# Optimization experiments

Hardware: AMD Instinct MI355X
Metric: run time of the kernel (lower is better)

The kernel has to match this reference:

```python
import jax, jax.numpy as jnp
import numpy as np

B, N, D, H = 2, 2048, 1024, 16
DK = D // H


def setup_inputs() -> dict:
    key = jax.random.key(0)
    ks = jax.random.split(key, 12)
    s = D ** -0.5
    inp = {
        "query": jax.random.normal(ks[0], (B, N, D), jnp.float32),
        "key": jax.random.normal(ks[1], (B, N, D), jnp.float32),
        "value": jax.random.normal(ks[2], (B, N, D), jnp.float32),
        # causal mask: 1 = keep, 0 = masked (matches create_causal_mask)
        "mask": jnp.tril(jnp.ones((N, N), jnp.int32)),
        "Wq": jax.random.normal(ks[3], (D, D), jnp.float32) * s,
        "bq": jnp.zeros((D,), jnp.float32),
        "Wk": jax.random.normal(ks[4], (D, D), jnp.float32) * s,
        "bk": jnp.zeros((D,), jnp.float32),
        "Wv": jax.random.normal(ks[5], (D, D), jnp.float32) * s,
        "bv": jnp.zeros((D,), jnp.float32),
        "Wo": jax.random.normal(ks[6], (D, D), jnp.float32) * s,
        "bo": jnp.zeros((D,), jnp.float32),
    }
    return inp


def reference(query, key, value, mask, Wq, bq, Wk, bk, Wv, bv, Wo, bo):
    scale = DK ** -0.5
    # Linear projections (torch nn.Linear: x @ W.T + b), split into heads -> [B,H,N,DK]
    q = (query @ Wq.T + bq).reshape(B, N, H, DK).transpose(0, 2, 1, 3)
    k = (key @ Wk.T + bk).reshape(B, N, H, DK).transpose(0, 2, 1, 3)
    v = (value @ Wv.T + bv).reshape(B, N, H, DK).transpose(0, 2, 1, 3)
    scores = jnp.einsum("bhqd,bhkd->bhqk", q, k) * scale  # [B,H,N,N]
    scores = jnp.where(mask[None, None, :, :] == 0, jnp.float32(-1e9), scores)
    attn = jax.nn.softmax(scores, axis=-1)
    ctx = jnp.einsum("bhqk,bhkd->bhqd", attn, v)  # [B,H,N,DK]
    ctx = ctx.transpose(0, 2, 1, 3).reshape(B, N, D)
    return ctx @ Wo.T + bo
```

## Files before the change

### kernel.cpp

```cpp
#include <hip/hip_runtime.h>
#include <hip/hip_bf16.h>

typedef __attribute__((ext_vector_type(4))) float f32x4;
typedef __attribute__((ext_vector_type(8))) __bf16 bf16x8;
typedef __attribute__((ext_vector_type(8))) unsigned short u16x8;
typedef __attribute__((ext_vector_type(4))) unsigned short u16x4;
typedef unsigned short u16;

#define DEV static __device__ __forceinline__

DEV u16 f2bf(float f){
  unsigned u = __builtin_bit_cast(unsigned, f);
  u += 0x7fff + ((u >> 16) & 1);
  return (u16)(u >> 16);
}

DEV f32x4 mfma16(bf16x8 a, bf16x8 b, f32x4 c){
  return __builtin_amdgcn_mfma_f32_16x16x32_bf16(a, b, c, 0, 0, 0);
}

DEV void gload16(const void* g, void* l){
  __builtin_amdgcn_global_load_lds((const __attribute__((address_space(1))) void*)g,
                                   (__attribute__((address_space(3))) void*)l,
                                   16, 0, 0);
}

__global__ __launch_bounds__(256) void cvt_k(
    const float* __restrict__ s0, const float* __restrict__ s1,
    const float* __restrict__ s2, const float* __restrict__ s3,
    const float* __restrict__ s4, const float* __restrict__ s5,
    const float* __restrict__ s6,
    u16* __restrict__ d0, u16* __restrict__ d1, u16* __restrict__ d2,
    u16* __restrict__ d3, u16* __restrict__ d4, u16* __restrict__ d5,
    u16* __restrict__ d6){
  const int y = blockIdx.y;
  const float* __restrict__ s = y==0?s0:y==1?s1:y==2?s2:y==3?s3:y==4?s4:y==5?s5:s6;
  u16* __restrict__ d         = y==0?d0:y==1?d1:y==2?d2:y==3?d3:y==4?d4:y==5?d5:d6;
  const int n8 = (y < 3) ? (4096*1024/8) : (1024*1024/8);
  for (int i = blockIdx.x*256 + threadIdx.x; i < n8; i += gridDim.x*256){
    f32x4 a = *(const f32x4*)&s[(size_t)i*8];
    f32x4 b = *(const f32x4*)&s[(size_t)i*8 + 4];
    u16x8 h;
    #pragma unroll
    for (int j = 0; j < 4; ++j){ h[j] = f2bf(a[j]); h[j+4] = f2bf(b[j]); }
    *(u16x8*)&d[(size_t)i*8] = h;
  }
}

template<int OUT_F32>
__global__ __launch_bounds__(256) void gemm_bt(
    const u16* __restrict__ A0, const u16* __restrict__ A1, const u16* __restrict__ A2,
    const u16* __restrict__ B0, const u16* __restrict__ B1, const u16* __restrict__ B2,
    const float* __restrict__ e0, const float* __restrict__ e1, const float* __restrict__ e2,
    void* __restrict__ C0, void* __restrict__ C1, void* __restrict__ C2){
  __shared__ u16 As[128*32];
  __shared__ u16 Bs[128*32];
  const int z = blockIdx.z;
  const u16* __restrict__ A    = z==0 ? A0 : z==1 ? A1 : A2;
  const u16* __restrict__ Bw   = z==0 ? B0 : z==1 ? B1 : B2;
  const float* __restrict__ bias = z==0 ? e0 : z==1 ? e1 : e2;
  void* __restrict__ Cp        = z==0 ? C0 : z==1 ? C1 : C2;
  const bool vt = (OUT_F32 == 0) && (z == 2);

  const int tid  = threadIdx.x;
  const int lane = tid & 63, w = tid >> 6;
  const int wr = w >> 1, wc = w & 1;
  const int l16 = lane & 15, lhi = lane >> 4;
  const int bm = vt ? blockIdx.x : blockIdx.y;
  const int bn = vt ? blockIdx.y : blockIdx.x;

  const int srow = w*16 + (lane >> 2);
  const int scol = (lane & 3)*8;
  const u16* Asrc = A  + (size_t)(bm*128 + srow)*1024 + scol;
  const u16* Bsrc = Bw + (size_t)(bn*128 + srow)*1024 + scol;
  u16* Adst0 = As + w*512;
  u16* Bdst0 = Bs + w*512;

  f32x4 acc[4][4] = {};

  for (int k0 = 0; k0 < 1024; k0 += 32){
    __syncthreads();
    gload16(Asrc + k0,             Adst0);
    gload16(Asrc + 64*1024 + k0,   Adst0 + 2048);
    gload16(Bsrc + k0,             Bdst0);
    gload16(Bsrc + 64*1024 + k0,   Bdst0 + 2048);
    __syncthreads();

    bf16x8 af[4], bfr[4];
    #pragma unroll
    for (int mi = 0; mi < 4; ++mi)
      af[mi] = *(const bf16x8*)&As[(wr*64 + mi*16 + l16)*32 + lhi*8];
    #pragma unroll
    for (int nf = 0; nf < 4; ++nf)
      bfr[nf] = *(const bf16x8*)&Bs[(wc*64 + nf*16 + l16)*32 + lhi*8];
    #pragma unroll
    for (int mi = 0; mi < 4; ++mi)
      #pragma unroll
      for (int nf = 0; nf < 4; ++nf)
        acc[mi][nf] = mfma16(af[mi], bfr[nf], acc[mi][nf]);
  }

  #pragma unroll
  for (int mi = 0; mi < 4; ++mi){
    #pragma unroll
    for (int nf = 0; nf < 4; ++nf){
      int row0 = bm*128 + wr*64 + mi*16 + lhi*4;
      int col  = bn*128 + wc*64 + nf*16 + l16;
      float bc = bias[col];
      #pragma unroll
      for (int r = 0; r < 4; ++r){
        int row = row0 + r;
        float val = acc[mi][nf][r] + (vt ? bias[row] : bc);
        if (OUT_F32){
          ((float*)Cp)[(size_t)row*1024 + col] = val;
        } else if (!vt){
          int b = row >> 11, n = row & 2047;
          int h = col >> 6,  dk = col & 63;
          ((u16*)Cp)[(((size_t)(b*16 + h))*2048 + n)*64 + dk] = f2bf(val);
        } else {
          int h = row >> 6,  dk = row & 63;
          int b = col >> 11, n = col & 2047;
          ((u16*)Cp)[(((size_t)(b*16 + h))*64 + dk)*2048 + n] = f2bf(val);
        }
      }
    }
  }
}

__global__ __launch_bounds__(256) void attn_k(const u16* __restrict__ Q,
                                              const u16* __restrict__ K,
                                              const u16* __restrict__ Vt,
                                              u16* __restrict__ CTX){
  __shared__ u16 Ks[64*64];
  __shared__ u16 Vs[64*64];
  __shared__ u16 Ps[4][16][72];
  const int tid  = threadIdx.x;
  const int lane = tid & 63, w = tid >> 6;
  const int l16 = lane & 15, lhi = lane >> 4;
  const int f  = blockIdx.x;
  const int bh = f & 31, xp = f >> 5;
  const size_t base = (size_t)bh * 2048 * 64;
  const u16* Qb = Q  + base;
  const u16* Kb = K  + base;
  const u16* Vb = Vt + base;
  const int b = bh >> 4, h = bh & 15;

  const int s0 = tid, s1 = tid + 256;
  const int r0 = s0 >> 3, c0 = ((s0 & 7) ^ (r0 & 7))*8;
  const int r1 = s1 >> 3, c1 = ((s1 & 7) ^ (r1 & 7))*8;
  const u16* Ksrc0 = Kb + r0*64 + c0;
  const u16* Ksrc1 = Kb + r1*64 + c1;
  const u16* Vsrc0 = Vb + (size_t)r0*2048 + c0;
  const u16* Vsrc1 = Vb + (size_t)r1*2048 + c1;
  u16* Kdst0 = Ks + s0*8;  u16* Kdst1 = Ks + s1*8;
  u16* Vdst0 = Vs + s0*8;  u16* Vdst1 = Vs + s1*8;
  const int swz = (l16 & 7)*8;

  #pragma unroll
  for (int half = 0; half < 2; ++half){
    const int qt = half == 0 ? xp : 31 - xp;
    const int q0 = qt * 64;
    const int q_abs = q0 + w*16 + l16;

    bf16x8 bq[2];
    #pragma unroll
    for (int ks = 0; ks < 2; ++ks)
      bq[ks] = *(const bf16x8*)&Qb[(size_t)q_abs*64 + ks*32 + lhi*8];

    f32x4 ctx[4] = {};
    float m_r = -3.0e38f, l_r = 0.f;

    const int nt = qt + 1;
    for (int t = 0; t < nt; ++t){
      __syncthreads();
      gload16(Ksrc0 + t*4096, Kdst0);
      gload16(Ksrc1 + t*4096, Kdst1);
      gload16(Vsrc0 + t*64,   Vdst0);
      gload16(Vsrc1 + t*64,   Vdst1);
      __syncthreads();

      f32x4 s4[4] = {};
      #pragma unroll
      for (int nf = 0; nf < 4; ++nf)
        #pragma unroll
        for (int ks = 0; ks < 2; ++ks){
          bf16x8 ak = *(const bf16x8*)&Ks[(nf*16 + l16)*64 + ((ks*32 + lhi*8) ^ swz)];
          s4[nf] = mfma16(ak, bq[ks], s4[nf]);
        }

      float mt = -3.0e38f;
      #pragma unroll
      for (int nf = 0; nf < 4; ++nf)
        #pragma unroll
        for (int r = 0; r < 4; ++r){
          float x = s4[nf][r] * 0.125f;
          int kc = t*64 + nf*16 + lhi*4 + r;
          x = (kc > q_abs) ? -1.0e30f : x;
          s4[nf][r] = x;
          mt = fmaxf(mt, x);
        }
      mt = fmaxf(mt, __shfl_xor(mt, 16));
      mt = fmaxf(mt, __shfl_xor(mt, 32));
      float mn = fmaxf(m_r, mt);
      float sf = __expf(m_r - mn);
      m_r = mn;

      float lt = 0.f;
      #pragma unroll
      for (int nf = 0; nf < 4; ++nf){
        u16x4 hq;
        #pragma unroll
        for (int r = 0; r < 4; ++r){
          float p = __expf(s4[nf][r] - mn);
          lt += p;
          hq[r] = f2bf(p);
        }
        *(u16x4*)&Ps[w][l16][nf*16 + lhi*4] = hq;
      }
      lt += __shfl_xor(lt, 16);
      lt += __shfl_xor(lt, 32);
      l_r = l_r * sf + lt;

      float sfb[4];
      #pragma unroll
      for (int r = 0; r < 4; ++r)
        sfb[r] = __shfl(sf, (lane >> 4)*4 + r);
      #pragma unroll
      for (int dkf = 0; dkf < 4; ++dkf)
        #pragma unroll
        for (int r = 0; r < 4; ++r)
          ctx[dkf][r] *= sfb[r];

      #pragma unroll
      for (int ks = 0; ks < 2; ++ks){
        bf16x8 pa = *(const bf16x8*)&Ps[w][l16][ks*32 + lhi*8];
        #pragma unroll
        for (int dkf = 0; dkf < 4; ++dkf){
          bf16x8 vb = *(const bf16x8*)&Vs[(dkf*16 + l16)*64 + ((ks*32 + lhi*8) ^ swz)];
          ctx[dkf] = mfma16(pa, vb, ctx[dkf]);
        }
      }
    }

    float lf[4];
    #pragma unroll
    for (int r = 0; r < 4; ++r)
      lf[r] = __shfl(l_r, (lane >> 4)*4 + r);
    #pragma unroll
    for (int dkf = 0; dkf < 4; ++dkf)
      #pragma unroll
      for (int r = 0; r < 4; ++r){
        int q = q0 + w*16 + lhi*4 + r;
        float val = ctx[dkf][r] / lf[r];
        CTX[((size_t)(b*2048 + q))*1024 + h*64 + dkf*16 + l16] = f2bf(val);
      }
  }
}

constexpr int LDP = 40;

__global__ __launch_bounds__(256) void gemm_qkv(
    const float* __restrict__ Aq, const float* __restrict__ Ak, const float* __restrict__ Av,
    const float* __restrict__ Bq, const float* __restrict__ Bk, const float* __restrict__ Bv,
    const float* __restrict__ eq, const float* __restrict__ ek, const float* __restrict__ ev,
    u16* __restrict__ Oq, u16* __restrict__ Ok, u16* __restrict__ Ov){
  __shared__ u16 As[128][LDP];
  __shared__ u16 Bs[128][LDP];
  const int z = blockIdx.z;
  const float* __restrict__ A   = z == 0 ? Aq : z == 1 ? Ak : Av;
  const float* __restrict__ W   = z == 0 ? Bq : z == 1 ? Bk : Bv;
  const float* __restrict__ bias= z == 0 ? eq : z == 1 ? ek : ev;
  u16* __restrict__ C           = z == 0 ? Oq : z == 1 ? Ok : Ov;
  const bool vt = (z == 2);

  const int tid  = threadIdx.x;
  const int lane = tid & 63, wv = tid >> 6;
  const int wr = wv >> 1, wc = wv & 1;
  const int l16 = lane & 15, lhi = lane >> 4;
  const int bm = vt ? blockIdx.x : blockIdx.y;
  const int bn = vt ? blockIdx.y : blockIdx.x;
  const int K = 1024;

  f32x4 acc[4][4] = {};

  for (int k0 = 0; k0 < K; k0 += 32){
    __syncthreads();
    #pragma unroll
    for (int j = 0; j < 4; ++j){
      int s = tid + j*256;
      int row = s >> 3, c4 = s & 7;
      f32x4 v = *(const f32x4*)&A[(size_t)(bm*128 + row)*K + k0 + c4*4];
      u16x4 hh;
      #pragma unroll
      for (int i = 0; i < 4; ++i) hh[i] = f2bf(v[i]);
      *(u16x4*)&As[row][c4*4] = hh;
    }
    #pragma unroll
    for (int j = 0; j < 4; ++j){
      int s = tid + j*256;
      int row = s >> 3, c4 = s & 7;
      f32x4 v = *(const f32x4*)&W[(size_t)(bn*128 + row)*K + k0 + c4*4];
      u16x4 hh;
      #pragma unroll
      for (int i = 0; i < 4; ++i) hh[i] = f2bf(v[i]);
      *(u16x4*)&Bs[row][c4*4] = hh;
    }
    __syncthreads();

    bf16x8 af[4], bfr[4];
    #pragma unroll
    for (int mi = 0; mi < 4; ++mi)
      af[mi] = *(const bf16x8*)&As[wr*64 + mi*16 + l16][lhi*8];
    #pragma unroll
    for (int nf = 0; nf < 4; ++nf)
      bfr[nf] = *(const bf16x8*)&Bs[wc*64 + nf*16 + l16][lhi*8];
    #pragma unroll
    for (int mi = 0; mi < 4; ++mi)
      #pragma unroll
      for (int nf = 0; nf < 4; ++nf)
        acc[mi][nf] = mfma16(af[mi], bfr[nf], acc[mi][nf]);
  }

  #pragma unroll
  for (int mi = 0; mi < 4; ++mi){
    #pragma unroll
    for (int nf = 0; nf < 4; ++nf){
      int row0 = bm*128 + wr*64 + mi*16 + lhi*4;
      int col  = bn*128 + wc*64 + nf*16 + l16;
      float bc = bias[col];
      #pragma unroll
      for (int r = 0; r < 4; ++r){
        int row = row0 + r;
        float val = acc[mi][nf][r] + (vt ? bias[row] : bc);
        if (!vt){
          int b = row >> 11, n = row & 2047;
          int h = col >> 6,  dk = col & 63;
          C[(((size_t)(b*16 + h))*2048 + n)*64 + dk] = f2bf(val);
        } else {
          int h = row >> 6,  dk = row & 63;
          int b = col >> 11, n = col & 2047;
          C[(((size_t)(b*16 + h))*64 + dk)*2048 + n] = f2bf(val);
        }
      }
    }
  }
}

__global__ __launch_bounds__(256) void gemm_o_fb(const u16* __restrict__ A,
                                                 const float* __restrict__ W,
                                                 const float* __restrict__ bias,
                                                 float* __restrict__ C){
  __shared__ u16 As[128][LDP];
  __shared__ u16 Bs[64][LDP];
  const int tid  = threadIdx.x;
  const int lane = tid & 63, wv = tid >> 6;
  const int wr = wv >> 1, wc = wv & 1;
  const int l16 = lane & 15, lhi = lane >> 4;
  const int bm = blockIdx.y, bn = blockIdx.x;
  const int K = 1024;

  f32x4 acc[4][2] = {};

  for (int k0 = 0; k0 < K; k0 += 32){
    __syncthreads();
    #pragma unroll
    for (int j = 0; j < 2; ++j){
      int s = tid + j*256;
      int row = s >> 2, c8 = s & 3;
      *(u16x8*)&As[row][c8*8] =
          *(const u16x8*)&A[(size_t)(bm*128 + row)*K + k0 + c8*8];
    }
    #pragma unroll
    for (int j = 0; j < 2; ++j){
      int s = tid + j*256;
      int row = s >> 3, c4 = s & 7;
      f32x4 v = *(const f32x4*)&W[(size_t)(bn*64 + row)*K + k0 + c4*4];
      u16x4 hh;
      #pragma unroll
      for (int i = 0; i < 4; ++i) hh[i] = f2bf(v[i]);
      *(u16x4*)&Bs[row][c4*4] = hh;
    }
    __syncthreads();

    bf16x8 af[4], bfr[2];
    #pragma unroll
    for (int mi = 0; mi < 4; ++mi)
      af[mi] = *(const bf16x8*)&As[wr*64 + mi*16 + l16][lhi*8];
    #pragma unroll
    for (int nf = 0; nf < 2; ++nf)
      bfr[nf] = *(const bf16x8*)&Bs[wc*32 + nf*16 + l16][lhi*8];
    #pragma unroll
    for (int mi = 0; mi < 4; ++mi)
      #pragma unroll
      for (int nf = 0; nf < 2; ++nf)
        acc[mi][nf] = mfma16(af[mi], bfr[nf], acc[mi][nf]);
  }

  #pragma unroll
  for (int mi = 0; mi < 4; ++mi){
    #pragma unroll
    for (int nf = 0; nf < 2; ++nf){
      int row0 = bm*128 + wr*64 + mi*16 + lhi*4;
      int col  = bn*64 + wc*32 + nf*16 + l16;
      float bv = bias[col];
      #pragma unroll
      for (int r = 0; r < 4; ++r)
        C[(size_t)(row0 + r)*1024 + col] = acc[mi][nf][r] + bv;
    }
  }
}

extern "C" void kernel_launch(void* const* d_in, const int* in_sizes, int n_in,
                              void* d_out, int out_size, void* d_ws, size_t ws_size,
                              hipStream_t stream){
  const float* q  = (const float*)d_in[0];
  const float* k  = (const float*)d_in[1];
  const float* v  = (const float*)d_in[2];
  const float* Wq = (const float*)d_in[4];  const float* bq = (const float*)d_in[5];
  const float* Wk = (const float*)d_in[6];  const float* bk = (const float*)d_in[7];
  const float* Wv = (const float*)d_in[8];  const float* bv = (const float*)d_in[9];
  const float* Wo = (const float*)d_in[10]; const float* bo = (const float*)d_in[11];
  float* out = (float*)d_out;
  dim3 blk(256);

  const size_t need = (size_t)(3*4194304 + 4*1048576 + 3*4194304) * 2;
  if (ws_size >= need){
    u16* Xqb = (u16*)d_ws;
    u16* Xkb = Xqb + 4194304;
    u16* Xvb = Xkb + 4194304;
    u16* Wqb = Xvb + 4194304;
    u16* Wkb = Wqb + 1048576;
    u16* Wvb = Wkb + 1048576;
    u16* Wob = Wvb + 1048576;
    u16* Qw  = Wob + 1048576;
    u16* Kw  = Qw + 4194304;
    u16* Vw  = Kw + 4194304;
    u16* Cw  = Xqb;

    cvt_k<<<dim3(512, 7), blk, 0, stream>>>(q, k, v, Wq, Wk, Wv, Wo,
                                            Xqb, Xkb, Xvb, Wqb, Wkb, Wvb, Wob);
    gemm_bt<0><<<dim3(8, 32, 3), blk, 0, stream>>>(
        Xqb, Xkb, Wvb, Wqb, Wkb, Xvb, bq, bk, bv,
        (void*)Qw, (void*)Kw, (void*)Vw);
    attn_k<<<dim3(512), blk, 0, stream>>>(Qw, Kw, Vw, Cw);
    gemm_bt<1><<<dim3(8, 32, 1), blk, 0, stream>>>(
        Cw, Cw, Cw, Wob, Wob, Wob, bo, bo, bo,
        (void*)out, (void*)out, (void*)out);
  } else {
    u16* Qw = (u16*)d_ws;
    u16* Kw = Qw + (size_t)4096*1024;
    u16* Vw = Kw + (size_t)4096*1024;
    u16* Cw = Vw + (size_t)4096*1024;
    gemm_qkv<<<dim3(8, 32, 3), blk, 0, stream>>>(q, k, Wv, Wq, Wk, v, bq, bk, bv,
                                                 Qw, Kw, Vw);
    attn_k<<<dim3(512), blk, 0, stream>>>(Qw, Kw, Vw, Cw);
    gemm_o_fb<<<dim3(16, 32), blk, 0, stream>>>(Cw, Wo, bo, out);
  }
}
```

Baseline: 143.0 us.

## Double-buffer K/V tiles and share them across both query tiles in attention

The attention kernel now processes its two query tiles (xp and 31-xp) together, so each K/V tile is loaded once and used by both. Loads are double-buffered: the next tile is issued before computing the current one, leaving one barrier per iteration instead of two. It also uses exp2 with a prescaled log2e factor, applies the causal mask only on the diagonal tile, and skips the max rescale unless the new max exceeds the old by a threshold. It truncates P to bf16 instead of rounding and sums the truncated values. This roughly doubles LDS use and register pressure.

```diff
diff --git a/kernel.cpp b/kernel.cpp
--- a/kernel.cpp
+++ b/kernel.cpp
@@ -23,6 +23,14 @@
   __builtin_amdgcn_global_load_lds((const __attribute__((address_space(1))) void*)g,
                                    (__attribute__((address_space(3))) void*)l,
                                    16, 0, 0);
+}
+
+DEV float fexp2(float x){
+#if __has_builtin(__builtin_amdgcn_exp2f)
+  return __builtin_amdgcn_exp2f(x);
+#else
+  float r; asm("v_exp_f32 %0, %1" : "=v"(r) : "v"(x)); return r;
+#endif
 }
 
 __global__ __launch_bounds__(256) void cvt_k(
@@ -127,13 +135,93 @@
   }
 }
 
+#define SCL 0.18033688011f
+#define THR 11.0f
+#define PLD 72
+
+DEV void proc_tile(int t, int qt, int q_abs,
+                   const u16* __restrict__ Ksb, const u16* __restrict__ Vsb,
+                   u16* __restrict__ PsW,
+                   bf16x8 bq0, bf16x8 bq1,
+                   f32x4* ctx, float& m_r, float& l_r,
+                   int l16, int lhi, int lane, int swz){
+  f32x4 s4[4] = {};
+  #pragma unroll
+  for (int nf = 0; nf < 4; ++nf){
+    bf16x8 ak0 = *(const bf16x8*)&Ksb[(nf*16 + l16)*64 + ((lhi*8) ^ swz)];
+    bf16x8 ak1 = *(const bf16x8*)&Ksb[(nf*16 + l16)*64 + ((32 + lhi*8) ^ swz)];
+    s4[nf] = mfma16(ak0, bq0, s4[nf]);
+    s4[nf] = mfma16(ak1, bq1, s4[nf]);
+  }
+
+  const bool domask = (t == qt);
+  float mt = -3.0e38f;
+  #pragma unroll
+  for (int nf = 0; nf < 4; ++nf)
+    #pragma unroll
+    for (int r = 0; r < 4; ++r){
+      float x = s4[nf][r] * SCL;
+      if (domask){
+        int kc = t*64 + nf*16 + lhi*4 + r;
+        x = (kc > q_abs) ? -1.0e30f : x;
+      }
+      s4[nf][r] = x;
+      mt = fmaxf(mt, x);
+    }
+  mt = fmaxf(mt, __shfl_xor(mt, 16));
+  mt = fmaxf(mt, __shfl_xor(mt, 32));
+
+  if (!__all(mt <= m_r + THR)){
+    float mn = fmaxf(m_r, mt);
+    float sf = fexp2(m_r - mn);
+    m_r = mn;
+    l_r *= sf;
+    float sfb[4];
+    #pragma unroll
+    for (int r = 0; r < 4; ++r)
+      sfb[r] = __shfl(sf, (lane >> 4)*4 + r);
+    #pragma unroll
+    for (int dkf = 0; dkf < 4; ++dkf)
+      #pragma unroll
+      for (int r = 0; r < 4; ++r)
+        ctx[dkf][r] *= sfb[r];
+  }
+
+  float lt = 0.f;
+  #pragma unroll
+  for (int nf = 0; nf < 4; ++nf){
+    u16x4 hq;
+    #pragma unroll
+    for (int r = 0; r < 4; ++r){
+      float p = fexp2(s4[nf][r] - m_r);
+      unsigned u = __builtin_bit_cast(unsigned, p) & 0xffff0000u;
+      lt += __builtin_bit_cast(float, u);
+      hq[r] = (u16)(u >> 16);
+    }
+    *(u16x4*)&PsW[l16*PLD + nf*16 + lhi*4] = hq;
+  }
+  lt += __shfl_xor(lt, 16);
+  lt += __shfl_xor(lt, 32);
+  l_r += lt;
+
+  #pragma unroll
+  for (int ks = 0; ks < 2; ++ks){
+    bf16x8 pa = *(const bf16x8*)&PsW[l16*PLD + ks*32 + lhi*8];
+    #pragma unroll
+    for (int dkf = 0; dkf < 4; ++dkf){
+      bf16x8 vb = *(const bf16x8*)&Vsb[(dkf*16 + l16)*64 + ((ks*32 + lhi*8) ^ swz)];
+      ctx[dkf] = mfma16(pa, vb, ctx[dkf]);
+    }
+  }
+}
+
 __global__ __launch_bounds__(256) void attn_k(const u16* __restrict__ Q,
                                               const u16* __restrict__ K,
                                               const u16* __restrict__ Vt,
                                               u16* __restrict__ CTX){
-  __shared__ u16 Ks[64*64];
-  __shared__ u16 Vs[64*64];
-  __shared__ u16 Ps[4][16][72];
+  __shared__ u16 Ks[2][64*64];
+  __shared__ u16 Vs[2][64*64];
+  __shared__ u16 Ps[4][2][16*PLD];
   const int tid  = threadIdx.x;
   const int lane = tid & 63, w = tid >> 6;
   const int l16 = lane & 15, lhi = lane >> 4;
@@ -152,109 +240,74 @@
   const u16* Ksrc1 = Kb + r1*64 + c1;
   const u16* Vsrc0 = Vb + (size_t)r0*2048 + c0;
   const u16* Vsrc1 = Vb + (size_t)r1*2048 + c1;
-  u16* Kdst0 = Ks + s0*8;  u16* Kdst1 = Ks + s1*8;
-  u16* Vdst0 = Vs + s0*8;  u16* Vdst1 = Vs + s1*8;
   const int swz = (l16 & 7)*8;
 
-  #pragma unroll
-  for (int half = 0; half < 2; ++half){
-    const int qt = half == 0 ? xp : 31 - xp;
-    const int q0 = qt * 64;
-    const int q_abs = q0 + w*16 + l16;
-
-    bf16x8 bq[2];
-    #pragma unroll
-    for (int ks = 0; ks < 2; ++ks)
-      bq[ks] = *(const bf16x8*)&Qb[(size_t)q_abs*64 + ks*32 + lhi*8];
-
-    f32x4 ctx[4] = {};
-    float m_r = -3.0e38f, l_r = 0.f;
-
-    const int nt = qt + 1;
-    for (int t = 0; t < nt; ++t){
-      __syncthreads();
-      gload16(Ksrc0 + t*4096, Kdst0);
-      gload16(Ksrc1 + t*4096, Kdst1);
-      gload16(Vsrc0 + t*64,   Vdst0);
-      gload16(Vsrc1 + t*64,   Vdst1);
-      __syncthreads();
-
-      f32x4 s4[4] = {};
-      #pragma unroll
-      for (int nf = 0; nf < 4; ++nf)
-        #pragma unroll
-        for (int ks = 0; ks < 2; ++ks){
-          bf16x8 ak = *(const bf16x8*)&Ks[(nf*16 + l16)*64 + ((ks*32 + lhi*8) ^ swz)];
-          s4[nf] = mfma16(ak, bq[ks], s4[nf]);
-        }
-
-      float mt = -3.0e38f;
-      #pragma unroll
-      for (int nf = 0; nf < 4; ++nf)
-        #pragma unroll
-        for (int r = 0; r < 4; ++r){
-          float x = s4[nf][r] * 0.125f;
-          int kc = t*64 + nf*16 + lhi*4 + r;
-          x = (kc > q_abs) ? -1.0e30f : x;
-          s4[nf][r] = x;
-          mt = fmaxf(mt, x);
-        }
-      mt = fmaxf(mt, __shfl_xor(mt, 16));
-      mt = fmaxf(mt, __shfl_xor(mt, 32));
-      float mn = fmaxf(m_r, mt);
-      float sf = __expf(m_r - mn);
-      m_r = mn;
-
-      float lt = 0.f;
-      #pragma unroll
-      for (int nf = 0; nf < 4; ++nf){
-        u16x4 hq;
-        #pragma unroll
-        for (int r = 0; r < 4; ++r){
-          float p = __expf(s4[nf][r] - mn);
-          lt += p;
-          hq[r] = f2bf(p);
-        }
-        *(u16x4*)&Ps[w][l16][nf*16 + lhi*4] = hq;
-      }
-      lt += __shfl_xor(lt, 16);
-      lt += __shfl_xor(lt, 32);
-      l_r = l_r * sf + lt;
-
-      float sfb[4];
-      #pragma unroll
-      for (int r = 0; r < 4; ++r)
-        sfb[r] = __shfl(sf, (lane >> 4)*4 + r);
-      #pragma unroll
-      for (int dkf = 0; dkf < 4; ++dkf)
-        #pragma unroll
-        for (int r = 0; r < 4; ++r)
-          ctx[dkf][r] *= sfb[r];
-
-      #pragma unroll
-      for (int ks = 0; ks < 2; ++ks){
-        bf16x8 pa = *(const bf16x8*)&Ps[w][l16][ks*32 + lhi*8];
-        #pragma unroll
-        for (int dkf = 0; dkf < 4; ++dkf){
-          bf16x8 vb = *(const bf16x8*)&Vs[(dkf*16 + l16)*64 + ((ks*32 + lhi*8) ^ swz)];
-          ctx[dkf] = mfma16(pa, vb, ctx[dkf]);
-        }
-      }
-    }
-
-    float lf[4];
-    #pragma unroll
-    for (int r = 0; r < 4; ++r)
-      lf[r] = __shfl(l_r, (lane >> 4)*4 + r);
-    #pragma unroll
-    for (int dkf = 0; dkf < 4; ++dkf)
-      #pragma unroll
-      for (int r = 0; r < 4; ++r){
-        int q = q0 + w*16 + lhi*4 + r;
-        float val = ctx[dkf][r] / lf[r];
-        CTX[((size_t)(b*2048 + q))*1024 + h*64 + dkf*16 + l16] = f2bf(val);
-      }
-  }
+  const int qtA = xp,      ntA = xp + 1;
+  const int qtB = 31 - xp, ntB = 32 - xp;
+  const int qaA = qtA*64 + w*16 + l16;
+  const int qaB = qtB*64 + w*16 + l16;
+
+  bf16x8 bqA0 = *(const bf16x8*)&Qb[(size_t)qaA*64 + lhi*8];
+  bf16x8 bqA1 = *(const bf16x8*)&Qb[(size_t)qaA*64 + 32 + lhi*8];
+  bf16x8 bqB0 = *(const bf16x8*)&Qb[(size_t)qaB*64 + lhi*8];
+  bf16x8 bqB1 = *(const bf16x8*)&Qb[(size_t)qaB*64 + 32 + lhi*8];
+
+  f32x4 ctxA[4] = {}, ctxB[4] = {};
+  float mA = -3.0e38f, lA = 0.f, mB = -3.0e38f, lB = 0.f;
+
+  u16* PsA = &Ps[w][0][0];
+  u16* PsB = &Ps[w][1][0];
+
+  gload16(Ksrc0, &Ks[0][s0*8]);  gload16(Ksrc1, &Ks[0][s1*8]);
+  gload16(Vsrc0, &Vs[0][s0*8]);  gload16(Vsrc1, &Vs[0][s1*8]);
+  __syncthreads();
+
+  int cur = 0;
+  int t = 0;
+  for (; t < ntA; ++t){
+    if (t + 1 < ntB){
+      int nb = cur ^ 1;
+      gload16(Ksrc0 + (t+1)*4096, &Ks[nb][s0*8]);
+      gload16(Ksrc1 + (t+1)*4096, &Ks[nb][s1*8]);
+      gload16(Vsrc0 + (t+1)*64,   &Vs[nb][s0*8]);
+      gload16(Vsrc1 + (t+1)*64,   &Vs[nb][s1*8]);
+    }
+    proc_tile(t, qtB, qaB, Ks[cur], Vs[cur], PsB, bqB0, bqB1,
+              ctxB, mB, lB, l16, lhi, lane, swz);
+    proc_tile(t, qtA, qaA, Ks[cur], Vs[cur], PsA, bqA0, bqA1,
+              ctxA, mA, lA, l16, lhi, lane, swz);
+    __syncthreads();
+    cur ^= 1;
+  }
+  for (; t < ntB; ++t){
+    if (t + 1 < ntB){
+      int nb = cur ^ 1;
+      gload16(Ksrc0 + (t+1)*4096, &Ks[nb][s0*8]);
+      gload16(Ksrc1 + (t+1)*4096, &Ks[nb][s1*8]);
+      gload16(Vsrc0 + (t+1)*64,   &Vs[nb][s0*8]);
+      gload16(Vsrc1 + (t+1)*64,   &Vs[nb][s1*8]);
+    }
+    proc_tile(t, qtB, qaB, Ks[cur], Vs[cur], PsB, bqB0, bqB1,
+              ctxB, mB, lB, l16, lhi, lane, swz);
+    __syncthreads();
+    cur ^= 1;
+  }
+
+  float lfA[4], lfB[4];
+  #pragma unroll
+  for (int r = 0; r < 4; ++r){
+    lfA[r] = __shfl(lA, (lane >> 4)*4 + r);
+    lfB[r] = __shfl(lB, (lane >> 4)*4 + r);
+  }
+  #pragma unroll
+  for (int dkf = 0; dkf < 4; ++dkf)
+    #pragma unroll
+    for (int r = 0; r < 4; ++r){
+      int qA = qtA*64 + w*16 + lhi*4 + r;
+      int qB = qtB*64 + w*16 + lhi*4 + r;
+      CTX[((size_t)(b*2048 + qA))*1024 + h*64 + dkf*16 + l16] = f2bf(ctxA[dkf][r] / lfA[r]);
+      CTX[((size_t)(b*2048 + qB))*1024 + h*64 + dkf*16 + l16] = f2bf(ctxB[dkf][r] / lfB[r]);
+    }
 }
 
 constexpr int LDP = 40;
```

After: 137.3 us. 4.0% less time.
